# Kernel optimization log

Hardware: AMD Instinct MI355X
Metric: run time of the kernel (lower is better)

## Reference

```python
import jax, jax.numpy as jnp
import numpy as np

VOCAB = 50000
WORD_DIM = 300
HIDDEN = 300
REL = 3
B = 512        # batch of (premise, hypothesis) tree pairs
LEAVES = 256   # leaves per complete binary tree (depth 8)


def setup_inputs() -> dict:
    key = jax.random.key(0)
    ks = jax.random.split(key, 6)
    sc = lambda k, shape, s: jax.random.normal(k, shape, dtype=jnp.float32) * s
    return {
        "word_ids": jax.random.randint(ks[0], (B, 2, LEAVES), 0, VOCAB),
        "embedding": sc(ks[1], (VOCAB, WORD_DIM), 0.1),
        "W_leaf": sc(ks[2], (HIDDEN, WORD_DIM), 0.05),   # word2hidden (no bias)
        "W_h": sc(ks[3], (HIDDEN, 2 * HIDDEN), 0.05),    # hidden2hidden
        "b_h": jnp.zeros((HIDDEN,), jnp.float32),
        "W_cls": sc(ks[4], (REL, 2 * HIDDEN), 0.05),
        "b_cls": jnp.zeros((REL,), jnp.float32),
    }


def _encode_trees(word_ids, embedding, W_leaf, W_h, b_h):
    # word_ids: [B, 2, L] leaf token ids of complete binary trees.
    # Leaf: h = word2hidden(embedding(id))  (no bias, no activation)
    h = embedding[word_ids] @ W_leaf.T                     # [B, 2, L, H]
    # Postorder combine, level-synchronous: parent = hidden2hidden(cat(l, r))
    n = h.shape[2]
    while n > 1:
        left = h[:, :, 0::2, :]
        right = h[:, :, 1::2, :]
        h = jnp.concatenate([left, right], axis=-1) @ W_h.T + b_h
        n //= 2
    return h[:, :, 0, :]                                   # [B, 2, H] roots


def reference(word_ids, embedding, W_leaf, W_h, b_h, W_cls, b_cls):
    roots = _encode_trees(word_ids, embedding, W_leaf, W_h, b_h)  # [B, 2, H]
    feat = jax.nn.sigmoid(roots.reshape(roots.shape[0], -1))      # cat(p, h) -> [B, 2H]
    logits = feat @ W_cls.T + b_cls                               # [B, REL]
    return jax.nn.log_softmax(logits, axis=-1)
```

## Files before the change

kernel.cpp:

```cpp
#include <hip/hip_runtime.h>
#include <hip/hip_bf16.h>

typedef __hip_bfloat16 bf16;
typedef __attribute__((ext_vector_type(8))) short short8;
typedef __attribute__((ext_vector_type(4))) float float4v;
typedef __attribute__((ext_vector_type(4))) short short4v;

__device__ __forceinline__ short f2bs(float x) {
    bf16 b = __float2bfloat16(x);
    return *reinterpret_cast<short*>(&b);
}
__device__ __forceinline__ float bs2f(short s) {
    bf16 b = *reinterpret_cast<bf16*>(&s);
    return __bfloat162float(b);
}

#define GLL16(g, l) __builtin_amdgcn_global_load_lds(                      \
    (const __attribute__((address_space(1))) void*)(g),                    \
    (__attribute__((address_space(3))) void*)(l), 16, 0, 0)

__global__ __launch_bounds__(256) void conv_all(
    const float* __restrict__ emb, const float* __restrict__ W_h,
    const float* __restrict__ W_leaf, const float* __restrict__ b_h,
    short* __restrict__ emb_bf, short* __restrict__ Bh,
    short* __restrict__ Bleaf, float* __restrict__ biasp)
{
    const int idx = blockIdx.x * 256 + threadIdx.x;
    if (idx < 4014080) {
        const int row = idx / 80;
        const int k4  = (idx - row * 80) * 4;
        short4v v = (short4v)0;
        if (row < 50000 && k4 < 300) {
            const float4v f = *reinterpret_cast<const float4v*>(
                emb + (long)row * 300 + k4);
#pragma unroll
            for (int j = 0; j < 4; ++j) v[j] = f2bs(f[j]);
        }
        *(short4v*)&emb_bf[(long)row * 320 + k4] = v;
        return;
    }
    const int j = idx - 4014080;
    if (j < 204800) {
        const int row = j / 640, k = j - row * 640;
        float v = 0.f;
        if (row < 300) {
            if (k < 300)                  v = W_h[row * 600 + k];
            else if (k >= 320 && k < 620) v = W_h[row * 600 + k - 20];
        }
        Bh[j] = f2bs(v);
    } else if (j < 307200) {
        const int i = j - 204800;
        const int row = i / 320, k = i - row * 320;
        Bleaf[i] = (row < 300 && k < 300) ? f2bs(W_leaf[row * 300 + k])
                                          : (short)0;
    } else if (j < 307520) {
        const int i = j - 307200;
        biasp[i] = (i < 300) ? b_h[i] : 0.f;
    }
}

template <int KE, int GMODE, bool BIAS>
__global__ __launch_bounds__(256, 2) void mfma_gemm(
    const short* __restrict__ Xsrc, const int* __restrict__ wid,
    const short* __restrict__ emb, const short* __restrict__ Wp,
    const float* __restrict__ biasp, short* __restrict__ out)
{
    static_assert(GMODE != 2 || KE == 640, "pair-gather requires KE=640");
    __shared__ __align__(16) short As[2][128 * 32];
    __shared__ __align__(16) short Bs[2][320 * 32];

    const int tid  = threadIdx.x;
    const int lane = tid & 63;
    const int w    = tid >> 6;
    const int wm   = w >> 1, wn = w & 1;
    const long m0  = (long)blockIdx.x * 128;

    const int s_q   = lane & 3;
    const int r_off = lane >> 2;

    const char* gL[2];
    const char* gR[2];
#pragma unroll
    for (int j = 0; j < 2; ++j) {
        const int r = (w * 2 + j) * 16 + r_off;
        const int q = s_q ^ ((r >> 1) & 3);
        if (GMODE == 2) {
            const long node = m0 + r;
            gL[j] = (const char*)emb + (long)wid[2 * node]     * 640 + q * 16;
            gR[j] = (const char*)emb + (long)wid[2 * node + 1] * 640 + q * 16;
        } else {
            gL[j] = (const char*)Xsrc + (m0 + r) * (long)(KE * 2) + q * 16;
            gR[j] = gL[j];
        }
    }
    const char* gB[5];
#pragma unroll
    for (int j = 0; j < 5; ++j) {
        const int r = (w * 5 + j) * 16 + r_off;
        const int q = s_q ^ ((r >> 1) & 3);
        gB[j] = (const char*)Wp + r * (long)(KE * 2) + q * 16;
    }

    int oA[4];
#pragma unroll
    for (int t = 0; t < 4; ++t) {
        const int row = wm * 64 + t * 16 + (lane & 15);
        const int s   = (lane >> 4) ^ ((row >> 1) & 3);
        oA[t] = row * 32 + s * 8;
    }
    int oB[10];
#pragma unroll
    for (int u = 0; u < 10; ++u) {
        const int n = wn * 160 + u * 16 + (lane & 15);
        const int s = (lane >> 4) ^ ((n >> 1) & 3);
        oB[u] = n * 32 + s * 8;
    }

    auto stage = [&](int buf, int kc) {
        char* baseA = (char*)&As[buf][0];
        char* baseB = (char*)&Bs[buf][0];
        if (GMODE == 2) {
            const bool lft = (kc < 10);
            const int off = (lft ? kc : kc - 10) * 64;
            GLL16((lft ? gL[0] : gR[0]) + off, baseA + (w * 2 + 0) * 1024);
            GLL16((lft ? gL[1] : gR[1]) + off, baseA + (w * 2 + 1) * 1024);
        } else {
            const int off = kc * 64;
            GLL16(gL[0] + off, baseA + (w * 2 + 0) * 1024);
            GLL16(gL[1] + off, baseA + (w * 2 + 1) * 1024);
        }
        const int offb = kc * 64;
#pragma unroll
        for (int j = 0; j < 5; ++j)
            GLL16(gB[j] + offb, baseB + (w * 5 + j) * 1024);
    };

    float4v acc[4][10];
#pragma unroll
    for (int t = 0; t < 4; ++t)
#pragma unroll
        for (int u = 0; u < 10; ++u) acc[t][u] = (float4v)0.f;

    const int NCH = KE / 32;
    stage(0, 0);
    for (int kc = 0; kc < NCH; ++kc) {
        const int cur = kc & 1;
        if (kc + 1 < NCH) {
            stage(cur ^ 1, kc + 1);
            asm volatile("s_waitcnt vmcnt(7)" ::: "memory");
        } else {
            asm volatile("s_waitcnt vmcnt(0)" ::: "memory");
        }
        __builtin_amdgcn_s_barrier();
        __builtin_amdgcn_sched_barrier(0);

        const short* bA = &As[cur][0];
        const short* bB = &Bs[cur][0];
        short8 a[4], b[10];
#pragma unroll
        for (int t = 0; t < 4; ++t) a[t] = *(const short8*)(bA + oA[t]);
#pragma unroll
        for (int u = 0; u < 10; ++u) b[u] = *(const short8*)(bB + oB[u]);
#pragma unroll
        for (int u = 0; u < 10; ++u)
#pragma unroll
            for (int t = 0; t < 4; ++t)
                acc[t][u] = __builtin_amdgcn_mfma_f32_16x16x32_bf16(
                    a[t], b[u], acc[t][u], 0, 0, 0);
        __builtin_amdgcn_s_barrier();
    }

#pragma unroll
    for (int u = 0; u < 10; ++u) {
        const int c = wn * 160 + u * 16 + (lane & 15);
        const float bv = BIAS ? biasp[c] : 0.f;
#pragma unroll
        for (int t = 0; t < 4; ++t) {
            const long mb = m0 + wm * 64 + t * 16 + (lane >> 4) * 4;
#pragma unroll
            for (int r4 = 0; r4 < 4; ++r4)
                out[(mb + r4) * 320 + c] = f2bs(acc[t][u][r4] + bv);
        }
    }
}

template<int MA, bool STREAM, bool TOROOTS>
__device__ __forceinline__ void tree_level(
    const int w, const int wl, const int lane,
    const short* Ain, short* Aout, short* Bs,
    const short* myAst, short* Ast0, short* Ast1,
    const char* gA0, const char* gA1,
    const char* gB0, const char* gB1, const char* gB2,
    const char* gB3, const char* gB4, const float* __restrict__ biasp)
{
    constexpr int MT  = (MA + 15) / 16;
    constexpr int TPW = MT * 5;
    const int lrow = lane & 15;
    const int hi   = lane >> 4;

    float4v acc[TPW];
#pragma unroll
    for (int t = 0; t < TPW; ++t) acc[t] = (float4v)0.f;

    for (int kc = 0; kc < 20; ++kc) {
        if (w < 4) {
            GLL16(gB0 + kc * 64, (char*)Bs + (w * 5 + 0) * 1024);
            GLL16(gB1 + kc * 64, (char*)Bs + (w * 5 + 1) * 1024);
            GLL16(gB2 + kc * 64, (char*)Bs + (w * 5 + 2) * 1024);
            GLL16(gB3 + kc * 64, (char*)Bs + (w * 5 + 3) * 1024);
            GLL16(gB4 + kc * 64, (char*)Bs + (w * 5 + 4) * 1024);
        } else if (STREAM) {
            const int off = (kc >= 10 ? 640 : 0) + (kc % 10) * 64;
            GLL16(gA0 + off, (char*)Ast0 + (w - 4) * 1024);
            GLL16(gA1 + off, (char*)Ast1 + (w - 4) * 1024);
        }
        asm volatile("s_waitcnt vmcnt(0)" ::: "memory");
        __builtin_amdgcn_s_barrier();
        __builtin_amdgcn_sched_barrier(0);

#pragma unroll
        for (int t = 0; t < TPW; ++t) {
            const int g  = wl + t * 4;
            const int mt = g / 20, nt = g % 20;
            int row = mt * 16 + lrow;
            if (MA < 16) row = (lrow < MA) ? lrow : 0;
            const int sa = hi ^ ((row >> 1) & 3);
            const short* pa = STREAM
                ? (myAst + row * 32 + sa * 8)
                : (Ain + kc * (MA * 32) + row * 32 + sa * 8);
            const int n  = nt * 16 + lrow;
            const int sb = hi ^ ((n >> 1) & 3);
            const short8 a = *(const short8*)pa;
            const short8 b = *(const short8*)(Bs + n * 32 + sb * 8);
            acc[t] = __builtin_amdgcn_mfma_f32_16x16x32_bf16(
                a, b, acc[t], 0, 0, 0);
        }
        __builtin_amdgcn_s_barrier();
    }

#pragma unroll
    for (int t = 0; t < TPW; ++t) {
        const int g  = wl + t * 4;
        const int mt = g / 20, nt = g % 20;
        const int c  = nt * 16 + lrow;
        const float bv = biasp[c];
#pragma unroll
        for (int r4 = 0; r4 < 4; ++r4) {
            const int mb = mt * 16 + hi * 4 + r4;
            if (mb < MA) {
                const short v = f2bs(acc[t][r4] + bv);
                if (TOROOTS) {
                    Aout[mb * 320 + c] = v;
                } else {
                    constexpr int MN = MA / 2;
                    const int p  = (mb & 1) * 10 + (c >> 5);
                    const int m2 = mb >> 1;
                    const int q  = (c >> 3) & 3;
                    Aout[p * (MN * 32) + m2 * 32 +
                         (q ^ ((m2 >> 1) & 3)) * 8 + (c & 7)] = v;
                }
            }
        }
    }
    __syncthreads();
}

__global__ __launch_bounds__(512, 1) void subtree(
    const short* __restrict__ L2in, const short* __restrict__ Wp,
    const float* __restrict__ biasp, const float* __restrict__ W_cls,
    const float* __restrict__ b_cls, float* __restrict__ outp)
{
    __shared__ __align__(16) short Bs[320 * 32];
    __shared__ __align__(16) short AXs[2][20 * 32 * 32];
    __shared__ __align__(16) short AYs[2][10240];
    __shared__ __align__(16) short Ast[2][2048];

    const int tid  = threadIdx.x;
    const int lane = tid & 63;
    const int w    = tid >> 6;
    const int wl   = w & 3;
    const int grp  = w >> 2;
    const int s_q   = lane & 3;
    const int r_off = lane >> 2;

    const char* gB[5];
#pragma unroll
    for (int j = 0; j < 5; ++j) {
        const int r = (wl * 5 + j) * 16 + r_off;
        const int q = s_q ^ ((r >> 1) & 3);
        gB[j] = (const char*)Wp + r * 1280L + q * 16;
    }
    const int wa = (w >= 4) ? (w - 4) : 0;
    const int rS = wa * 16 + r_off;
    const int qS = s_q ^ ((rS >> 1) & 3);
    const long base0 = (long)(2 * blockIdx.x) * 128;
    const char* gA0 = (const char*)L2in + (base0 + 2 * rS) * 640 + qS * 16;
    const char* gA1 = (const char*)L2in + (base0 + 128 + 2 * rS) * 640 + qS * 16;

    short* AXm = AXs[grp];
    short* AYm = AYs[grp];

    tree_level<64, true,  false>(w, wl, lane, nullptr, AXm, Bs,
                                 Ast[grp], Ast[0], Ast[1], gA0, gA1,
                                 gB[0], gB[1], gB[2], gB[3], gB[4], biasp);
    tree_level<32, false, false>(w, wl, lane, AXm, AYm, Bs,
                                 nullptr, nullptr, nullptr, nullptr, nullptr,
                                 gB[0], gB[1], gB[2], gB[3], gB[4], biasp);
    tree_level<16, false, false>(w, wl, lane, AYm, AXm, Bs,
                                 nullptr, nullptr, nullptr, nullptr, nullptr,
                                 gB[0], gB[1], gB[2], gB[3], gB[4], biasp);
    tree_level<8,  false, false>(w, wl, lane, AXm, AYm, Bs,
                                 nullptr, nullptr, nullptr, nullptr, nullptr,
                                 gB[0], gB[1], gB[2], gB[3], gB[4], biasp);
    tree_level<4,  false, false>(w, wl, lane, AYm, AXm, Bs,
                                 nullptr, nullptr, nullptr, nullptr, nullptr,
                                 gB[0], gB[1], gB[2], gB[3], gB[4], biasp);
    tree_level<2,  false, true >(w, wl, lane, AXm, AYm, Bs,
                                 nullptr, nullptr, nullptr, nullptr, nullptr,
                                 gB[0], gB[1], gB[2], gB[3], gB[4], biasp);

    if (wl == 0) {
        const short* rowp = AYs[grp];
        float a0 = 0.f, a1 = 0.f, a2 = 0.f;
#pragma unroll
        for (int i = 0; i < 10; ++i) {
            const int k = lane + 64 * i;
            if (k < 600) {
                const int col = (k < 300) ? k : (320 + k - 300);
                const float f = 1.f / (1.f + __expf(-bs2f(rowp[col])));
                a0 += f * W_cls[k];
                a1 += f * W_cls[600 + k];
                a2 += f * W_cls[1200 + k];
            }
        }
#pragma unroll
        for (int off = 32; off > 0; off >>= 1) {
            a0 += __shfl_down(a0, off);
            a1 += __shfl_down(a1, off);
            a2 += __shfl_down(a2, off);
        }
        if (lane == 0) {
            const int b = blockIdx.x * 2 + grp;
            const float l0 = a0 + b_cls[0];
            const float l1 = a1 + b_cls[1];
            const float l2 = a2 + b_cls[2];
            const float m  = fmaxf(l0, fmaxf(l1, l2));
            const float s  = __expf(l0 - m) + __expf(l1 - m) + __expf(l2 - m);
            const float ls = m + __logf(s);
            outp[b * 3 + 0] = l0 - ls;
            outp[b * 3 + 1] = l1 - ls;
            outp[b * 3 + 2] = l2 - ls;
        }
    }
}

extern "C" void kernel_launch(void* const* d_in, const int* in_sizes, int n_in,
                              void* d_out, int out_size, void* d_ws, size_t ws_size,
                              hipStream_t stream)
{
    const int*   wid    = (const int*)d_in[0];
    const float* emb    = (const float*)d_in[1];
    const float* W_leaf = (const float*)d_in[2];
    const float* W_h    = (const float*)d_in[3];
    const float* b_h    = (const float*)d_in[4];
    const float* W_cls  = (const float*)d_in[5];
    const float* b_cls  = (const float*)d_in[6];
    float* outp = (float*)d_out;

    (void)in_sizes; (void)n_in; (void)out_size; (void)ws_size;

    char* ws = (char*)d_ws;
    short* bufA   = (short*)(ws);
    short* bufB   = (short*)(ws + 83886080);
    short* emb_bf = (short*)(ws + 83886080);
    short* Hv     = (short*)(ws + 125829120);
    short* Bleaf  = (short*)(ws + 157941760);
    short* Bh     = (short*)(ws + 158146560);
    float* biasp  = (float*)(ws + 158556160);

    conv_all<<<(4321600 + 255) / 256, 256, 0, stream>>>(
        emb, W_h, W_leaf, b_h, emb_bf, Bh, Bleaf, biasp);

    mfma_gemm<320, 0, false><<<50176 / 128, 256, 0, stream>>>(
        emb_bf, nullptr, nullptr, Bleaf, biasp, Hv);

    mfma_gemm<640, 2, true><<<131072 / 128, 256, 0, stream>>>(
        nullptr, wid, Hv, Bh, biasp, bufA);

    mfma_gemm<640, 0, true><<<65536 / 128, 256, 0, stream>>>(
        bufA, nullptr, nullptr, Bh, biasp, bufB);

    subtree<<<256, 512, 0, stream>>>(bufB, Bh, biasp, W_cls, b_cls, outp);
}
```

Measured before the change: 304.0 us.

## Double-buffer weight and streamed-input LDS tiles in subtree kernel levels

Splits the shared B-weight tile and the streamed level-input tile into two buffers so the next K-chunk's global-to-LDS loads are issued before computing on the current chunk, waiting with partial vmcnt. This aims to hide global load latency behind MFMA work in each tree level. The streamed-input staging now reuses the AY buffers, which are otherwise unused during the first level, to stay within the LDS budget. LDS use still grows because the B tile doubles.

Measured after the change: 293.5 us. 3.5% less time.

```diff
diff --git a/kernel.cpp b/kernel.cpp
--- a/kernel.cpp
+++ b/kernel.cpp
@@ -187,7 +187,7 @@
 template<int MA, bool STREAM, bool TOROOTS>
 __device__ __forceinline__ void tree_level(
     const int w, const int wl, const int lane,
-    const short* Ain, short* Aout, short* Bs,
+    const short* Ain, short* Aout, short* Bs0, short* Bs1,
     const short* myAst, short* Ast0, short* Ast1,
     const char* gA0, const char* gA1,
     const char* gB0, const char* gB1, const char* gB2,
@@ -202,22 +202,35 @@
 #pragma unroll
     for (int t = 0; t < TPW; ++t) acc[t] = (float4v)0.f;
 
-    for (int kc = 0; kc < 20; ++kc) {
+    auto stage = [&](int buf, int kc) {
         if (w < 4) {
-            GLL16(gB0 + kc * 64, (char*)Bs + (w * 5 + 0) * 1024);
-            GLL16(gB1 + kc * 64, (char*)Bs + (w * 5 + 1) * 1024);
-            GLL16(gB2 + kc * 64, (char*)Bs + (w * 5 + 2) * 1024);
-            GLL16(gB3 + kc * 64, (char*)Bs + (w * 5 + 3) * 1024);
-            GLL16(gB4 + kc * 64, (char*)Bs + (w * 5 + 4) * 1024);
+            char* base = (char*)(buf ? Bs1 : Bs0);
+            GLL16(gB0 + kc * 64, base + (w * 5 + 0) * 1024);
+            GLL16(gB1 + kc * 64, base + (w * 5 + 1) * 1024);
+            GLL16(gB2 + kc * 64, base + (w * 5 + 2) * 1024);
+            GLL16(gB3 + kc * 64, base + (w * 5 + 3) * 1024);
+            GLL16(gB4 + kc * 64, base + (w * 5 + 4) * 1024);
         } else if (STREAM) {
             const int off = (kc >= 10 ? 640 : 0) + (kc % 10) * 64;
-            GLL16(gA0 + off, (char*)Ast0 + (w - 4) * 1024);
-            GLL16(gA1 + off, (char*)Ast1 + (w - 4) * 1024);
-        }
-        asm volatile("s_waitcnt vmcnt(0)" ::: "memory");
+            GLL16(gA0 + off, (char*)Ast0 + buf * 4096 + (w - 4) * 1024);
+            GLL16(gA1 + off, (char*)Ast1 + buf * 4096 + (w - 4) * 1024);
+        }
+    };
+
+    stage(0, 0);
+    for (int kc = 0; kc < 20; ++kc) {
+        const int cur = kc & 1;
+        if (kc + 1 < 20) {
+            stage(cur ^ 1, kc + 1);
+            if (w < 4)       asm volatile("s_waitcnt vmcnt(5)" ::: "memory");
+            else if (STREAM) asm volatile("s_waitcnt vmcnt(2)" ::: "memory");
+        } else {
+            asm volatile("s_waitcnt vmcnt(0)" ::: "memory");
+        }
         __builtin_amdgcn_s_barrier();
         __builtin_amdgcn_sched_barrier(0);
 
+        const short* Bsc = cur ? Bs1 : Bs0;
 #pragma unroll
         for (int t = 0; t < TPW; ++t) {
             const int g  = wl + t * 4;
@@ -226,12 +239,12 @@
             if (MA < 16) row = (lrow < MA) ? lrow : 0;
             const int sa = hi ^ ((row >> 1) & 3);
             const short* pa = STREAM
-                ? (myAst + row * 32 + sa * 8)
+                ? (myAst + cur * 2048 + row * 32 + sa * 8)
                 : (Ain + kc * (MA * 32) + row * 32 + sa * 8);
             const int n  = nt * 16 + lrow;
             const int sb = hi ^ ((n >> 1) & 3);
             const short8 a = *(const short8*)pa;
-            const short8 b = *(const short8*)(Bs + n * 32 + sb * 8);
+            const short8 b = *(const short8*)(Bsc + n * 32 + sb * 8);
             acc[t] = __builtin_amdgcn_mfma_f32_16x16x32_bf16(
                 a, b, acc[t], 0, 0, 0);
         }
@@ -270,10 +283,9 @@
     const float* __restrict__ biasp, const float* __restrict__ W_cls,
     const float* __restrict__ b_cls, float* __restrict__ outp)
 {
-    __shared__ __align__(16) short Bs[320 * 32];
+    __shared__ __align__(16) short Bs[2][320 * 32];
     __shared__ __align__(16) short AXs[2][20 * 32 * 32];
     __shared__ __align__(16) short AYs[2][10240];
-    __shared__ __align__(16) short Ast[2][2048];
 
     const int tid  = threadIdx.x;
     const int lane = tid & 63;
@@ -300,22 +312,22 @@
     short* AXm = AXs[grp];
     short* AYm = AYs[grp];
 
-    tree_level<64, true,  false>(w, wl, lane, nullptr, AXm, Bs,
-                                 Ast[grp], Ast[0], Ast[1], gA0, gA1,
-                                 gB[0], gB[1], gB[2], gB[3], gB[4], biasp);
-    tree_level<32, false, false>(w, wl, lane, AXm, AYm, Bs,
+    tree_level<64, true,  false>(w, wl, lane, nullptr, AXm, Bs[0], Bs[1],
+                                 AYs[grp], AYs[0], AYs[1], gA0, gA1,
+                                 gB[0], gB[1], gB[2], gB[3], gB[4], biasp);
+    tree_level<32, false, false>(w, wl, lane, AXm, AYm, Bs[0], Bs[1],
                                  nullptr, nullptr, nullptr, nullptr, nullptr,
                                  gB[0], gB[1], gB[2], gB[3], gB[4], biasp);
-    tree_level<16, false, false>(w, wl, lane, AYm, AXm, Bs,
+    tree_level<16, false, false>(w, wl, lane, AYm, AXm, Bs[0], Bs[1],
                                  nullptr, nullptr, nullptr, nullptr, nullptr,
                                  gB[0], gB[1], gB[2], gB[3], gB[4], biasp);
-    tree_level<8,  false, false>(w, wl, lane, AXm, AYm, Bs,
+    tree_level<8,  false, false>(w, wl, lane, AXm, AYm, Bs[0], Bs[1],
                                  nullptr, nullptr, nullptr, nullptr, nullptr,
                                  gB[0], gB[1], gB[2], gB[3], gB[4], biasp);
-    tree_level<4,  false, false>(w, wl, lane, AYm, AXm, Bs,
+    tree_level<4,  false, false>(w, wl, lane, AYm, AXm, Bs[0], Bs[1],
                                  nullptr, nullptr, nullptr, nullptr, nullptr,
                                  gB[0], gB[1], gB[2], gB[3], gB[4], biasp);
-    tree_level<2,  false, true >(w, wl, lane, AXm, AYm, Bs,
+    tree_level<2,  false, true >(w, wl, lane, AXm, AYm, Bs[0], Bs[1],
                                  nullptr, nullptr, nullptr, nullptr, nullptr,
                                  gB[0], gB[1], gB[2], gB[3], gB[4], biasp);
 
```
